# Optimization experiments

Hardware: AMD Instinct MI355X
Metric: run time of the kernel (lower is better)

The kernel has to match this reference:

```python
import jax, jax.numpy as jnp
import numpy as np

VOCAB = 128000
D = 256
N_BUBBLES = 256
N_EQ_STEPS = 5
SEQ_LEN = 512
ETA = 0.1      # relaxation rate toward input
KAPPA = 0.05   # mean-field coupling between bubbles


def setup_inputs() -> dict:
    key = jax.random.key(0)
    k1, k2, k3 = jax.random.split(key, 3)
    embed = jax.random.normal(k1, (VOCAB, D), dtype=jnp.float32)
    bubbles = jax.random.normal(k2, (N_BUBBLES, D), dtype=jnp.float32)
    memory_decay_base = jnp.asarray(0.8, dtype=jnp.float32)
    novelty_sensitivity = jnp.asarray(1.0, dtype=jnp.float32)
    tokens = jax.random.randint(k3, (SEQ_LEN,), 0, VOCAB, dtype=jnp.int64)
    return {"embed": embed, "bubbles": bubbles,
            "memory_decay_base": memory_decay_base,
            "novelty_sensitivity": novelty_sensitivity,
            "tokens": tokens}


def _foam_forward(x, bubbles):
    """x: [d]. Equilibrate bubble states, build density matrix, eigen-spectrum."""
    s = bubbles  # [n_bubbles, d]
    for _ in range(N_EQ_STEPS):  # fixed small hyperparam loop
        s = s + ETA * (x[None, :] - s) + KAPPA * (s.mean(axis=0, keepdims=True) - s)
        s = s / (jnp.linalg.norm(s, axis=-1, keepdims=True) + 1e-10)
    rho = (s.T @ s) / s.shape[0]  # [d, d] PSD, trace ~ 1
    w = jnp.linalg.eigvalsh(rho)  # ascending eigenvalues [d]
    w = jnp.clip(w, 0.0)
    output_dist = w / (w.sum() + 1e-10)
    return s, output_dist


def reference(embed, bubbles, memory_decay_base, novelty_sensitivity, tokens):
    sens = jnp.abs(novelty_sensitivity)

    def step(memory, tok):
        x = embed[tok]                      # [d]
        mem_mean = memory.mean(axis=0)      # [d]
        mem_norm = jnp.linalg.norm(mem_mean) + 1e-10
        x_norm = jnp.linalg.norm(x) + 1e-10
        novelty = jnp.where(mem_norm > 1e-8,
                            1.0 - jnp.dot(x, mem_mean) / (x_norm * mem_norm),
                            1.0)
        decay = jax.nn.sigmoid(memory_decay_base - sens * novelty)
        x_with_memory = x + decay * mem_mean
        eq, output_dist = _foam_forward(x_with_memory, bubbles)
        memory = decay * memory + (1.0 - decay) * eq
        return memory, output_dist

    memory0 = jnp.zeros_like(bubbles)  # [n_bubbles, d]
    _, dists = jax.lax.scan(step, memory0, tokens)
    return dists  # [seq_len, d] per-step eigenvalue distributions of rho
```

## Files before the change

### kernel.cpp

```cpp
#include <hip/hip_runtime.h>
#include <hip/hip_fp16.h>
#include <math.h>

#define SEQ 512
#define ETA 0.1f
#define KAPPA 0.05f
#define AA 0.85f

typedef _Float16 f16x8 __attribute__((ext_vector_type(8)));
typedef float f32x4 __attribute__((ext_vector_type(4)));

#define WS_G    ((size_t)0)
#define WS_GD   ((size_t)65536)
#define WS_M0   ((size_t)65792)
#define WS_BX   ((size_t)66048)
#define WS_X2   ((size_t)197120)
#define WS_ZS   ((size_t)197632)
#define WS_YS   ((size_t)328704)
#define WS_GS   ((size_t)459776)
#define WS_HS   ((size_t)984064)
#define WS_ALS  ((size_t)986112)
#define WS_BETS ((size_t)1117184)
#define WS_CT   ((size_t)1772544)

__device__ __forceinline__ float wred_sum(float v) {
#pragma unroll
  for (int m = 1; m < 64; m <<= 1) v += __shfl_xor(v, m, 64);
  return v;
}
__device__ __forceinline__ float wred_min(float v) {
#pragma unroll
  for (int m = 1; m < 64; m <<= 1) v = fminf(v, __shfl_xor(v, m, 64));
  return v;
}
__device__ __forceinline__ float wred_max(float v) {
#pragma unroll
  for (int m = 1; m < 64; m <<= 1) v = fmaxf(v, __shfl_xor(v, m, 64));
  return v;
}
__device__ __forceinline__ float rfl(float x) {
  return __builtin_bit_cast(float, __builtin_amdgcn_readfirstlane(__builtin_bit_cast(int, x)));
}

__global__ void k0_gram(const float* __restrict__ B, float* __restrict__ ws) {
  float* G = ws + WS_G;
  float* Gd = ws + WS_GD;
  __shared__ float bi[256];
  const int i = blockIdx.x, j = threadIdx.x;
  bi[j] = B[(size_t)i * 256 + j];
  __syncthreads();
  float a0 = 0.f, a1 = 0.f, a2 = 0.f, a3 = 0.f;
#pragma unroll
  for (int c = 0; c < 256; c += 4) {
    float4 b4 = *(const float4*)&B[(size_t)j * 256 + c];
    a0 = fmaf(bi[c + 0], b4.x, a0);
    a1 = fmaf(bi[c + 1], b4.y, a1);
    a2 = fmaf(bi[c + 2], b4.z, a2);
    a3 = fmaf(bi[c + 3], b4.w, a3);
  }
  float acc = (a0 + a1) + (a2 + a3);
  G[(size_t)i * 256 + j] = acc;
  if (i == j) Gd[i] = acc;
}

__global__ void k0_m0(const float* __restrict__ B, float* __restrict__ ws) {
  float* M0 = ws + WS_M0;
  const int d = threadIdx.x;
  float acc = 0.f;
  for (int i = 0; i < 256; ++i) acc += B[(size_t)i * 256 + d];
  M0[d] = acc * (1.0f / 256.0f);
}

__global__ void k0_bx(const float* __restrict__ B, const float* __restrict__ embed,
                      const int* __restrict__ toks, float* __restrict__ ws) {
  float* BX = ws + WS_BX;
  float* X2 = ws + WS_X2;
  __shared__ float xs[256];
  __shared__ float red[4];
  const int t = blockIdx.x, i = threadIdx.x;
  const int lane = i & 63, wid = i >> 6;
  const int tok = toks[t];
  float xv = embed[(size_t)tok * 256 + i];
  xs[i] = xv;
  float p = wred_sum(xv * xv);
  if (lane == 0) red[wid] = p;
  __syncthreads();
  if (i == 0) X2[t] = red[0] + red[1] + red[2] + red[3];
  float a0 = 0.f, a1 = 0.f, a2 = 0.f, a3 = 0.f;
#pragma unroll
  for (int c = 0; c < 256; c += 4) {
    float4 b4 = *(const float4*)&B[(size_t)i * 256 + c];
    a0 = fmaf(xs[c + 0], b4.x, a0);
    a1 = fmaf(xs[c + 1], b4.y, a1);
    a2 = fmaf(xs[c + 2], b4.z, a2);
    a3 = fmaf(xs[c + 3], b4.w, a3);
  }
  BX[(size_t)t * 256 + i] = (a0 + a1) + (a2 + a3);
}

__global__ __launch_bounds__(1024, 1) void k1_seq(
    const float* __restrict__ embed, const int* __restrict__ toks,
    const float* __restrict__ mdbp, const float* __restrict__ sensp,
    float* __restrict__ ws) {
  const int tid = threadIdx.x;
  const int lane = tid & 63;
  const int i = tid >> 2, h = tid & 3;
  const float* G = ws + WS_G;
  const float* Gd = ws + WS_GD;
  const float* BX = ws + WS_BX;
  const float* X2 = ws + WS_X2;
  float* ZS = ws + WS_ZS;
  float* YS = ws + WS_YS;
  float* GS = ws + WS_GS;
  float* HS = ws + WS_HS;
  float* ALS = ws + WS_ALS;
  float* BETS = ws + WS_BETS;

  __shared__ __align__(16) float gcur[4 * 68];
  __shared__ float dresb[2][8];
  __shared__ float bbarb[2][8];

  float4 Gq[16];
  {
    const float4* gp = (const float4*)(G + (size_t)i * 256 + (size_t)h * 64);
#pragma unroll
    for (int j = 0; j < 16; ++j) Gq[j] = gp[j];
  }
  const float Gdi = Gd[i];
  const float mdb = rfl(mdbp[0]);
  const float sens = fabsf(rfl(sensp[0]));

  float q0i;
  {
    float s = 0.f;
#pragma unroll
    for (int j = 0; j < 16; ++j) s += (Gq[j].x + Gq[j].y) + (Gq[j].z + Gq[j].w);
    s += __shfl_xor(s, 1, 64);
    s += __shfl_xor(s, 2, 64);
    q0i = s * (1.0f / 256.0f);
  }

  float x_c = embed[(size_t)toks[0] * 256 + i];
  float bx_c = BX[i];
  float x2_c = rfl(X2[0]);

  if (tid < 16) dresb[tid >> 3][tid & 7] = 0.f;
  else if (tid < 32) bbarb[(tid - 16) >> 3][tid & 7] = 0.f;
  __syncthreads();
  {
    float mv0 = 0.f;
    if (h == 0) mv0 = q0i * (1.0f / 256.0f);
    else if (h == 1) mv0 = bx_c * (1.0f / 256.0f);
#pragma unroll
    for (int m = 4; m <= 32; m <<= 1) mv0 += __shfl_xor(mv0, m, 64);
    if (lane < 2) atomicAdd(&dresb[0][lane], mv0);
  }
  __syncthreads();
  const float c00 = rfl(dresb[0][0]);
  float mbx = rfl(dresb[0][1]);

  float Zi = 0.f, yi = 0.f, wi = 0.f;
  float mm2 = 0.f, mw = 0.f, dotxm = 0.f;

  float dec = 1.0f / (1.0f + expf(-(mdb - sens)));
  float od = 1.0f - dec;
  float ri = bx_c;
  float XM2 = x2_c;
  float mean_r = mbx;
  if (h == 0) ZS[i] = 0.f;
  else if (h == 1) YS[i] = x_c;

  float gh[6], Ggh[6], hhv[6], bmat[5], xmm[5], alpha;
  gh[0] = 1.0f / 256.0f; Ggh[0] = q0i; hhv[0] = 0.f;
  {
    const float xmm0 = mean_r;
    const float tki = ETA * ri + KAPPA * q0i;
    const float CC00 = (ETA * ETA) * XM2 + 2.f * (ETA * KAPPA) * xmm0 +
                       (KAPPA * KAPPA) * c00;
    const float n2 = fmaxf(AA * AA * Gdi + 2.f * AA * tki + CC00, 0.f);
    const float inv = 1.0f / (sqrtf(n2) + 1e-10f);
    bmat[0] = inv; alpha = AA * inv; xmm[0] = xmm0;
  }
  if (h == 0) gcur[(i >> 6) * 68 + (i & 63)] = alpha;
  {
    float bv0 = (h == 0) ? bmat[0] : 0.f;
#pragma unroll
    for (int m = 4; m <= 32; m <<= 1) bv0 += __shfl_xor(bv0, m, 64);
    if (lane == 0) atomicAdd(&bbarb[1][0], bv0);
  }
  __syncthreads();
  int pq = 1;

#pragma unroll 1
  for (int t = 0; t < SEQ; ++t) {
    const int tn = (t + 1 < SEQ) ? (t + 1) : t;
    const int tokn = toks[tn];
    const float x_n = embed[(size_t)tokn * 256 + i];
    const float bx_n = BX[(size_t)tn * 256 + i];
    const float x2_n = rfl(X2[tn]);
    float q5sav = 0.f;

#pragma unroll
    for (int k = 1; k <= 5; ++k) {
      if (tid < 8) dresb[1 - pq][tid] = 0.f;
      else if (tid < 16) bbarb[1 - pq][tid - 8] = 0.f;
      float4 av = {0.f, 0.f, 0.f, 0.f};
      const float4* gc4 = (const float4*)&gcur[h * 68];
#pragma unroll
      for (int j = 0; j < 16; ++j) {
        const float4 g4 = gc4[j];
        av.x = fmaf(Gq[j].x, g4.x, av.x);
        av.y = fmaf(Gq[j].y, g4.y, av.y);
        av.z = fmaf(Gq[j].z, g4.z, av.z);
        av.w = fmaf(Gq[j].w, g4.w, av.w);
      }
      float M = (av.x + av.y) + (av.z + av.w);
      M += __shfl_xor(M, 1, 64);
      M += __shfl_xor(M, 2, 64);
      float hk = 0.f, gk = alpha * (1.0f / 256.0f), Ggk = M * (1.0f / 256.0f);
#pragma unroll
      for (int l = 0; l < 5; ++l)
        if (l < k) {
          const float bb = rfl(bbarb[pq][l]) * (1.0f / 256.0f);
          hk += bb * (ETA + KAPPA * hhv[l]);
          gk = fmaf(KAPPA * bb, gh[l], gk);
          Ggk = fmaf(KAPPA * bb, Ggh[l], Ggk);
        }
      const float qk = Ggk + hk * ri;
      gh[k] = gk; Ggh[k] = Ggk; hhv[k] = hk;
      if (k <= 4) {
        if (h == 2) GS[(size_t)(k - 1) * (SEQ * 256) + (size_t)t * 256 + i] = gk;
        if (tid == 0) HS[(size_t)(k - 1) * SEQ + t] = hk;
      }
      float vv[8];
      if (k < 5) {
#pragma unroll
        for (int l = 0; l < 8; ++l) {
          if (l <= k) vv[l] = gk * (Ggh[l] + hhv[l] * ri);
          else if (l == k + 1) vv[l] = ri * gk;
          else vv[l] = 0.f;
        }
      } else {
        q5sav = qk;
        vv[0] = gk * qk;
        vv[1] = ri * gk;
        vv[2] = wi * gk;
        vv[3] = qk * (1.0f / 256.0f);
        vv[4] = bx_n * Zi + x_n * yi;
        vv[5] = bx_n * gk;
        vv[6] = x_n * x_c;
        vv[7] = bx_n * (1.0f / 256.0f);
      }
      float mv0 = (h == 0) ? vv[0] : (h == 1) ? vv[1] : (h == 2) ? vv[2] : vv[3];
      float mv1 = (h == 0) ? vv[4] : (h == 1) ? vv[5] : (h == 2) ? vv[6] : vv[7];
#pragma unroll
      for (int m = 4; m <= 32; m <<= 1) {
        mv0 += __shfl_xor(mv0, m, 64);
        mv1 += __shfl_xor(mv1, m, 64);
      }
      const int nv = (k < 5) ? (k + 2) : 8;
      if (lane < 8 && lane < nv) atomicAdd(&dresb[pq][lane], lane < 4 ? mv0 : mv1);
      __syncthreads();

      if (k < 5) {
        float dres[7];
#pragma unroll
        for (int l = 0; l < 7; ++l)
          if (l <= k + 1) dres[l] = rfl(dresb[pq][l]);
        const float xmmk = dres[k + 1] + hk * XM2;
        const float tki = ETA * ri + KAPPA * qk;
        float sc = alpha * tki;
#pragma unroll
        for (int jj = 0; jj < 4; ++jj)
          if (jj < k) {
            const float MMjk = dres[jj] + hk * xmm[jj];
            const float CCjk = (ETA * ETA) * XM2 + (ETA * KAPPA) * (xmm[jj] + xmmk) +
                               (KAPPA * KAPPA) * MMjk;
            sc = fmaf(bmat[jj], CCjk, sc);
          }
        const float MMkk = dres[k] + hk * xmmk;
        const float CCkk = (ETA * ETA) * XM2 + 2.f * (ETA * KAPPA) * xmmk +
                           (KAPPA * KAPPA) * MMkk;
        const float n2 = fmaxf(AA * AA + 2.f * AA * sc + CCkk, 0.f);
        const float inv = 1.0f / (sqrtf(n2) + 1e-10f);
#pragma unroll
        for (int jj = 0; jj < 4; ++jj)
          if (jj < k) bmat[jj] *= AA * inv;
        bmat[k] = inv;
        alpha *= AA * inv;
        xmm[k] = xmmk;
        if (k == 4) {
          if (h == 3) ALS[(size_t)t * 256 + i] = alpha;
          if (h == 0) {
            BETS[(size_t)0 * (SEQ * 256) + (size_t)t * 256 + i] = bmat[0];
            BETS[(size_t)4 * (SEQ * 256) + (size_t)t * 256 + i] = bmat[4];
          } else if (h == 1) {
            BETS[(size_t)1 * (SEQ * 256) + (size_t)t * 256 + i] = bmat[1];
          } else if (h == 2) {
            BETS[(size_t)2 * (SEQ * 256) + (size_t)t * 256 + i] = bmat[2];
          } else {
            BETS[(size_t)3 * (SEQ * 256) + (size_t)t * 256 + i] = bmat[3];
          }
        }
        if (h == 0) gcur[(i >> 6) * 68 + (i & 63)] = alpha;
        float bv0 = (h == 0) ? bmat[0]
                  : (h == 1) ? ((k >= 1) ? bmat[1] : 0.f)
                  : (h == 2) ? ((k >= 2) ? bmat[2] : 0.f)
                             : ((k >= 3) ? bmat[3] : 0.f);
        float bv1 = (h == 0 && k >= 4) ? bmat[4] : 0.f;
#pragma unroll
        for (int m = 4; m <= 32; m <<= 1) {
          bv0 += __shfl_xor(bv0, m, 64);
          bv1 += __shfl_xor(bv1, m, 64);
        }
        if (lane < 8 && lane <= k)
          atomicAdd(&bbarb[1 - pq][lane], lane < 4 ? bv0 : bv1);
        __syncthreads();
        pq ^= 1;
      } else {
        float dr[8];
#pragma unroll
        for (int l = 0; l < 8; ++l) dr[l] = rfl(dresb[pq][l]);
        const float h5 = hhv[5];
        const float g5 = gh[5];
        const float q5 = q5sav;
        const float xmm5 = dr[1] + h5 * XM2;
        const float m52 = dr[0] + h5 * xmm5;
        const float cmm5 = dr[2] + h5 * (dotxm + dec * mm2);
        const float lamc = dec * (1.0f + od * h5);
        Zi = lamc * Zi + od * g5;
        yi = lamc * yi + od * h5 * x_c;
        wi = dec * wi + od * q5;
        mm2 = fmaxf(dec * dec * mm2 + 2.f * dec * od * cmm5 + od * od * m52, 0.f);
        mw = dec * mw + od * dr[3];
        dotxm = lamc * dr[4] + od * (dr[5] + h5 * dr[6]);
        mbx = dr[7];
        x_c = x_n; bx_c = bx_n; x2_c = x2_n;
        const float memnorm = sqrtf(mm2) + 1e-10f;
        const float xnorm = sqrtf(x2_c) + 1e-10f;
        const float nov = (memnorm > 1e-8f) ? (1.0f - dotxm / (xnorm * memnorm)) : 1.0f;
        dec = 1.0f / (1.0f + expf(-(mdb - sens * nov)));
        od = 1.0f - dec;
        ri = bx_c + dec * wi;
        XM2 = x2_c + 2.f * dec * dotxm + dec * dec * mm2;
        mean_r = mbx + dec * mw;
        if (t + 1 < SEQ) {
          if (h == 0) ZS[(size_t)(t + 1) * 256 + i] = dec * Zi;
          else if (h == 1) YS[(size_t)(t + 1) * 256 + i] = x_c + dec * yi;
        }
        const float xmm0 = mean_r;
        const float tki = ETA * ri + KAPPA * q0i;
        const float CC00 = (ETA * ETA) * XM2 + 2.f * (ETA * KAPPA) * xmm0 +
                           (KAPPA * KAPPA) * c00;
        const float n2 = fmaxf(AA * AA * Gdi + 2.f * AA * tki + CC00, 0.f);
        const float inv = 1.0f / (sqrtf(n2) + 1e-10f);
        bmat[0] = inv; alpha = AA * inv; xmm[0] = xmm0;
        if (h == 0) gcur[(i >> 6) * 68 + (i & 63)] = alpha;
        float bv0 = (h == 0) ? bmat[0] : 0.f;
#pragma unroll
        for (int m = 4; m <= 32; m <<= 1) bv0 += __shfl_xor(bv0, m, 64);
        if (lane == 0) atomicAdd(&bbarb[1 - pq][0], bv0);
        __syncthreads();
        pq ^= 1;
      }
    }
  }
}

__global__ void k15_cvec(const float* __restrict__ B, float* __restrict__ ws) {
  const float* ZS = ws + WS_ZS;
  const float* YS = ws + WS_YS;
  const float* GS = ws + WS_GS;
  const float* HS = ws + WS_HS;
  const float* M0 = ws + WS_M0;
  float* CT = ws + WS_CT;
  const int t = blockIdx.x, d = threadIdx.x;
  __shared__ float zs[256], g1[256], g2[256], g3[256], g4[256];
  zs[d] = ZS[(size_t)t * 256 + d];
  g1[d] = GS[0 * (SEQ * 256) + (size_t)t * 256 + d];
  g2[d] = GS[1 * (SEQ * 256) + (size_t)t * 256 + d];
  g3[d] = GS[2 * (SEQ * 256) + (size_t)t * 256 + d];
  g4[d] = GS[3 * (SEQ * 256) + (size_t)t * 256 + d];
  __syncthreads();
  float xa = 0.f, b1 = 0.f, b2 = 0.f, b3 = 0.f, b4 = 0.f;
  for (int ii = 0; ii < 256; ++ii) {
    const float Bv = B[(size_t)ii * 256 + d];
    xa = fmaf(zs[ii], Bv, xa);
    b1 = fmaf(g1[ii], Bv, b1);
    b2 = fmaf(g2[ii], Bv, b2);
    b3 = fmaf(g3[ii], Bv, b3);
    b4 = fmaf(g4[ii], Bv, b4);
  }
  const float xm = YS[(size_t)t * 256 + d] + xa;
  float* ctt = CT + (size_t)t * 1280;
  ctt[0 * 256 + d] = ETA * xm + KAPPA * M0[d];
  const float h1 = HS[0 * SEQ + t], h2 = HS[1 * SEQ + t];
  const float h3 = HS[2 * SEQ + t], h4 = HS[3 * SEQ + t];
  ctt[1 * 256 + d] = (ETA + KAPPA * h1) * xm + KAPPA * b1;
  ctt[2 * 256 + d] = (ETA + KAPPA * h2) * xm + KAPPA * b2;
  ctt[3 * 256 + d] = (ETA + KAPPA * h3) * xm + KAPPA * b3;
  ctt[4 * 256 + d] = (ETA + KAPPA * h4) * xm + KAPPA * b4;
}

__global__ __launch_bounds__(1024, 4) void k2_eig(
    const float* __restrict__ B, const float* __restrict__ ws,
    float* __restrict__ out) {
  const int t = blockIdx.x;
  const int tid = threadIdx.x;
  const int lane = tid & 63, wid = tid >> 6;
  const float* CT = ws + WS_CT + (size_t)t * 1280;
  const float* ALS = ws + WS_ALS + (size_t)t * 256;
  const float* BETS = ws + WS_BETS;

  __shared__ __align__(16) unsigned char bigbuf[135168];
  _Float16* sT = (_Float16*)bigbuf;
  float* pk = (float*)bigbuf;
  __shared__ __align__(16) float ct[1280];
  __shared__ float vx[256], pv[256], qv[256];
  __shared__ float dd[256], ee[256], e2[256], lamv[256];
  __shared__ float red[16];

  for (int idx = tid; idx < 1280; idx += 1024) ct[idx] = CT[idx];
  __syncthreads();

  {
    const int r = tid >> 2, q = tid & 3;
    const float al = ALS[r];
    const float be0 = BETS[(size_t)0 * (SEQ * 256) + (size_t)t * 256 + r];
    const float be1 = BETS[(size_t)1 * (SEQ * 256) + (size_t)t * 256 + r];
    const float be2 = BETS[(size_t)2 * (SEQ * 256) + (size_t)t * 256 + r];
    const float be3 = BETS[(size_t)3 * (SEQ * 256) + (size_t)t * 256 + r];
    const float be4 = BETS[(size_t)4 * (SEQ * 256) + (size_t)t * 256 + r];
#pragma unroll
    for (int j4 = 0; j4 < 16; ++j4) {
      const int d0 = q * 64 + j4 * 4;
      const float4 Bv = *(const float4*)&B[(size_t)r * 256 + d0];
      const float4 c0 = *(const float4*)&ct[0 * 256 + d0];
      const float4 c1 = *(const float4*)&ct[1 * 256 + d0];
      const float4 c2 = *(const float4*)&ct[2 * 256 + d0];
      const float4 c3 = *(const float4*)&ct[3 * 256 + d0];
      const float4 c4 = *(const float4*)&ct[4 * 256 + d0];
      const float s0 = al * Bv.x + be0 * c0.x + be1 * c1.x + be2 * c2.x + be3 * c3.x + be4 * c4.x;
      const float s1 = al * Bv.y + be0 * c0.y + be1 * c1.y + be2 * c2.y + be3 * c3.y + be4 * c4.y;
      const float s2 = al * Bv.z + be0 * c0.z + be1 * c1.z + be2 * c2.z + be3 * c3.z + be4 * c4.z;
      const float s3 = al * Bv.w + be0 * c0.w + be1 * c1.w + be2 * c2.w + be3 * c3.w + be4 * c4.w;
      sT[(size_t)(d0 + 0) * 264 + r] = (_Float16)s0;
      sT[(size_t)(d0 + 1) * 264 + r] = (_Float16)s1;
      sT[(size_t)(d0 + 2) * 264 + r] = (_Float16)s2;
      sT[(size_t)(d0 + 3) * 264 + r] = (_Float16)s3;
    }
  }
  __syncthreads();

  f32x4 acc[4][4];
#pragma unroll
  for (int ti = 0; ti < 4; ++ti)
#pragma unroll
    for (int tj = 0; tj < 4; ++tj) {
      f32x4 z = {0.f, 0.f, 0.f, 0.f};
      acc[ti][tj] = z;
    }
  {
    const int Ib = (wid >> 2) * 4, Jb = (wid & 3) * 4;
    const int mr = lane & 15, kg = lane >> 4;
#pragma unroll 1
    for (int kb = 0; kb < 8; ++kb) {
      const int ko = kb * 32 + kg * 8;
      f16x8 aF[4], bF[4];
#pragma unroll
      for (int ti = 0; ti < 4; ++ti)
        aF[ti] = *(const f16x8*)&sT[(size_t)((Ib + ti) * 16 + mr) * 264 + ko];
#pragma unroll
      for (int tj = 0; tj < 4; ++tj)
        bF[tj] = *(const f16x8*)&sT[(size_t)((Jb + tj) * 16 + mr) * 264 + ko];
#pragma unroll
      for (int ti = 0; ti < 4; ++ti)
#pragma unroll
        for (int tj = 0; tj < 4; ++tj)
          acc[ti][tj] = __builtin_amdgcn_mfma_f32_16x16x32_f16(aF[ti], bF[tj], acc[ti][tj], 0, 0, 0);
    }
  }
  __syncthreads();
  {
    const int Ib = (wid >> 2) * 4, Jb = (wid & 3) * 4;
    const int cn = lane & 15, rg = lane >> 4;
#pragma unroll
    for (int ti = 0; ti < 4; ++ti)
#pragma unroll
      for (int tj = 0; tj < 4; ++tj) {
        const int C = (Jb + tj) * 16 + cn;
        const int Rb = (Ib + ti) * 16 + rg * 4;
#pragma unroll
        for (int rr = 0; rr < 4; ++rr) {
          const int R = Rb + rr;
          if (R >= C) pk[R * (R + 1) / 2 + C] = acc[ti][tj][rr] * (1.0f / 256.0f);
        }
      }
  }
  __syncthreads();

#pragma unroll 1
  for (int j = 0; j < 254; ++j) {
    const int m = 255 - j;
    const float x0 = pk[(j + 1) * (j + 2) / 2 + j];
    float ps = 0.f;
    if (tid < m) {
      const int gr = j + 1 + tid;
      const float xv_ = pk[gr * (gr + 1) / 2 + j];
      vx[tid] = xv_;
      ps = xv_ * xv_;
    }
    ps = wred_sum(ps);
    if (lane == 0) red[wid] = ps;
    __syncthreads();
    float sig2 = 0.f;
#pragma unroll
    for (int w = 0; w < 16; ++w) sig2 += red[w];
    const float sig = sqrtf(sig2);
    const float sg = (x0 >= 0.f) ? 1.f : -1.f;
    const bool live = (sig2 > 1e-26f);
    const float beta = live ? (1.0f / (sig * (sig + fabsf(x0)))) : 0.f;
    const float v0 = live ? (x0 + sg * sig) : 0.f;
    if (tid == 0) {
      dd[j] = pk[j * (j + 1) / 2 + j];
      ee[j] = live ? (-sg * sig) : x0;
      vx[0] = v0;
    }
    __syncthreads();
    {
      const int ri_ = tid >> 2, qd = tid & 3;
      float acc2 = 0.f;
      if (ri_ < m) {
        const int gr = j + 1 + ri_;
        const int c0 = (m * qd) >> 2, c1 = (m * (qd + 1)) >> 2;
        const int rowbase = gr * (gr + 1) / 2 + (j + 1);
        const int clend = min(c1, ri_ + 1);
        for (int c = c0; c < clend; ++c) acc2 = fmaf(pk[rowbase + c], vx[c], acc2);
        const int cu = max(c0, ri_ + 1);
        if (cu < c1) {
          int gc = j + 1 + cu;
          int ub = gc * (gc + 1) / 2 + gr;
          int stp = gc + 1;
          for (int c = cu; c < c1; ++c) { acc2 = fmaf(pk[ub], vx[c], acc2); ub += stp; ++stp; }
        }
      }
      acc2 += __shfl_xor(acc2, 1, 64);
      acc2 += __shfl_xor(acc2, 2, 64);
      float vpp = 0.f;
      if ((tid & 3) == 0 && (tid >> 2) < m) { pv[tid >> 2] = acc2; vpp = acc2 * vx[tid >> 2]; }
      vpp = wred_sum(vpp);
      if (lane == 0) red[wid] = vpp;
    }
    __syncthreads();
    float vtp = 0.f;
#pragma unroll
    for (int w = 0; w < 16; ++w) vtp += red[w];
    const float gamma = 0.5f * beta * beta * vtp;
    if (tid < m) qv[tid] = beta * pv[tid] - gamma * vx[tid];
    __syncthreads();
    {
      const int Q = tid >> 2, qd = tid & 3;
      const int i2 = m - 1 - Q;
      if (Q <= i2 && Q < m) {
        {
          const int gr = j + 1 + Q;
          const int rb = gr * (gr + 1) / 2 + (j + 1);
          const float vi = vx[Q], qi = qv[Q];
          const int cs = (qd * (Q + 1)) >> 2, ce = ((qd + 1) * (Q + 1)) >> 2;
          for (int c = cs; c < ce; ++c) pk[rb + c] -= vi * qv[c] + qi * vx[c];
        }
        if (i2 > Q) {
          const int gr = j + 1 + i2;
          const int rb = gr * (gr + 1) / 2 + (j + 1);
          const float vi = vx[i2], qi = qv[i2];
          const int cs = (qd * (i2 + 1)) >> 2, ce = ((qd + 1) * (i2 + 1)) >> 2;
          for (int c = cs; c < ce; ++c) pk[rb + c] -= vi * qv[c] + qi * vx[c];
        }
      }
    }
    __syncthreads();
  }
  if (tid == 0) {
    dd[254] = pk[254 * 255 / 2 + 254];
    dd[255] = pk[255 * 256 / 2 + 255];
    ee[254] = pk[255 * 256 / 2 + 254];
    ee[255] = 0.f;
  }
  __syncthreads();
  if (tid < 256) e2[tid] = ee[tid] * ee[tid];
  __syncthreads();
  float glo = 1e30f, ghi = -1e30f;
  if (tid < 256) {
    const float rad = fabsf(ee[tid]) + ((tid > 0) ? fabsf(ee[tid - 1]) : 0.f);
    glo = dd[tid] - rad;
    ghi = dd[tid] + rad;
  }
  {
    float v = wred_min(glo);
    if (lane == 0) red[wid] = v;
    __syncthreads();
    float lo0 = 1e30f;
#pragma unroll
    for (int w = 0; w < 16; ++w) lo0 = fminf(lo0, red[w]);
    __syncthreads();
    v = wred_max(ghi);
    if (lane == 0) red[wid] = v;
    __syncthreads();
    float hi0 = -1e30f;
#pragma unroll
    for (int w = 0; w < 16; ++w) hi0 = fmaxf(hi0, red[w]);
    lo0 -= 1e-3f + 1e-3f * fabsf(lo0);
    hi0 += 1e-3f + 1e-3f * fabsf(hi0);
    if (tid < 256) {
      float lo = lo0, hi = hi0;
      for (int it = 0; it < 21; ++it) {
        const float x = 0.5f * (lo + hi);
        int cnt = 0;
        float qq = dd[0] - x;
        cnt += (qq < 0.f);
        for (int ii = 1; ii < 256; ++ii) {
          float dn = qq;
          if (fabsf(dn) < 1e-25f) dn = (dn < 0.f) ? -1e-25f : 1e-25f;
          qq = (dd[ii] - x) - e2[ii - 1] * __builtin_amdgcn_rcpf(dn);
          cnt += (qq < 0.f);
        }
        if (cnt >= tid + 1) hi = x; else lo = x;
      }
      lamv[tid] = fmaxf(0.5f * (lo + hi), 0.f);
    }
  }
  __syncthreads();
  float sv = (tid < 256) ? lamv[tid] : 0.f;
  sv = wred_sum(sv);
  if (lane == 0) red[wid] = sv;
  __syncthreads();
  float S = 0.f;
#pragma unroll
  for (int w = 0; w < 16; ++w) S += red[w];
  if (tid < 256) out[(size_t)t * 256 + tid] = lamv[tid] / (S + 1e-10f);
}

extern "C" void kernel_launch(void* const* d_in, const int* in_sizes, int n_in,
                              void* d_out, int out_size, void* d_ws, size_t ws_size,
                              hipStream_t stream) {
  const float* embed = (const float*)d_in[0];
  const float* B = (const float*)d_in[1];
  const float* mdb = (const float*)d_in[2];
  const float* sens = (const float*)d_in[3];
  const int* toks = (const int*)d_in[4];
  float* out = (float*)d_out;
  float* ws = (float*)d_ws;

  k0_gram<<<dim3(256), dim3(256), 0, stream>>>(B, ws);
  k0_m0<<<dim3(1), dim3(256), 0, stream>>>(B, ws);
  k0_bx<<<dim3(SEQ), dim3(256), 0, stream>>>(B, embed, toks, ws);
  k1_seq<<<dim3(1), dim3(1024), 0, stream>>>(embed, toks, mdb, sens, ws);
  k15_cvec<<<dim3(SEQ), dim3(256), 0, stream>>>(B, ws);
  k2_eig<<<dim3(SEQ), dim3(1024), 0, stream>>>(B, ws, out);
}
```

Before: 12.01 ms.

## Halve sequential kernel block to 512 threads with two lanes per row

The single-block sequential recurrence kernel now runs 512 threads, with each row of the Gram matrix split across 2 threads instead of 4. Each thread holds 32 float4 registers of G, named through a macro so they stay in registers. This removes one shuffle level and cuts the number of waves taking part in each barrier. Reductions are rewritten as 32-lane partial sums whose results are combined with atomics. The cost is higher register pressure and more serial FMA work per thread in the matrix-vector product.

```diff
diff --git a/kernel.cpp b/kernel.cpp
--- a/kernel.cpp
+++ b/kernel.cpp
@@ -38,9 +38,22 @@
   for (int m = 1; m < 64; m <<= 1) v = fmaxf(v, __shfl_xor(v, m, 64));
   return v;
 }
+__device__ __forceinline__ float psum32(float v) {
+  v += __shfl_xor(v, 2, 64);
+  v += __shfl_xor(v, 4, 64);
+  v += __shfl_xor(v, 8, 64);
+  v += __shfl_xor(v, 16, 64);
+  v += __shfl_xor(v, 32, 64);
+  return v;
+}
 __device__ __forceinline__ float rfl(float x) {
   return __builtin_bit_cast(float, __builtin_amdgcn_readfirstlane(__builtin_bit_cast(int, x)));
 }
+
+#define G_LIST(X) X(0) X(1) X(2) X(3) X(4) X(5) X(6) X(7) \
+                  X(8) X(9) X(10) X(11) X(12) X(13) X(14) X(15) \
+                  X(16) X(17) X(18) X(19) X(20) X(21) X(22) X(23) \
+                  X(24) X(25) X(26) X(27) X(28) X(29) X(30) X(31)
 
 __global__ void k0_gram(const float* __restrict__ B, float* __restrict__ ws) {
   float* G = ws + WS_G;
@@ -98,13 +111,15 @@
   BX[(size_t)t * 256 + i] = (a0 + a1) + (a2 + a3);
 }
 
-__global__ __launch_bounds__(1024, 1) void k1_seq(
+__global__ __launch_bounds__(512)
+__attribute__((amdgpu_waves_per_eu(2, 2)))
+void k1_seq(
     const float* __restrict__ embed, const int* __restrict__ toks,
     const float* __restrict__ mdbp, const float* __restrict__ sensp,
     float* __restrict__ ws) {
   const int tid = threadIdx.x;
   const int lane = tid & 63;
-  const int i = tid >> 2, h = tid & 3;
+  const int i = tid >> 1, h = tid & 1;
   const float* G = ws + WS_G;
   const float* Gd = ws + WS_GD;
   const float* BX = ws + WS_BX;
@@ -116,16 +131,14 @@
   float* ALS = ws + WS_ALS;
   float* BETS = ws + WS_BETS;
 
-  __shared__ __align__(16) float gcur[4 * 68];
+  __shared__ __align__(16) float gcur[256];
   __shared__ float dresb[2][8];
   __shared__ float bbarb[2][8];
 
-  float4 Gq[16];
-  {
-    const float4* gp = (const float4*)(G + (size_t)i * 256 + (size_t)h * 64);
-#pragma unroll
-    for (int j = 0; j < 16; ++j) Gq[j] = gp[j];
-  }
+  const float4* gp = (const float4*)(G + (size_t)i * 256 + (size_t)h * 128);
+#define DECLG(J) float4 Gr##J = gp[J];
+  G_LIST(DECLG)
+#undef DECLG
   const float Gdi = Gd[i];
   const float mdb = rfl(mdbp[0]);
   const float sens = fabsf(rfl(sensp[0]));
@@ -133,10 +146,10 @@
   float q0i;
   {
     float s = 0.f;
-#pragma unroll
-    for (int j = 0; j < 16; ++j) s += (Gq[j].x + Gq[j].y) + (Gq[j].z + Gq[j].w);
+#define SUMG(J) s += (Gr##J.x + Gr##J.y) + (Gr##J.z + Gr##J.w);
+    G_LIST(SUMG)
+#undef SUMG
     s += __shfl_xor(s, 1, 64);
-    s += __shfl_xor(s, 2, 64);
     q0i = s * (1.0f / 256.0f);
   }
 
@@ -148,12 +161,9 @@
   else if (tid < 32) bbarb[(tid - 16) >> 3][tid & 7] = 0.f;
   __syncthreads();
   {
-    float mv0 = 0.f;
-    if (h == 0) mv0 = q0i * (1.0f / 256.0f);
-    else if (h == 1) mv0 = bx_c * (1.0f / 256.0f);
-#pragma unroll
-    for (int m = 4; m <= 32; m <<= 1) mv0 += __shfl_xor(mv0, m, 64);
-    if (lane < 2) atomicAdd(&dresb[0][lane], mv0);
+    float v = h ? (bx_c * (1.0f / 256.0f)) : (q0i * (1.0f / 256.0f));
+    v = psum32(v);
+    if (lane == h) atomicAdd(&dresb[0][h], v);
   }
   __syncthreads();
   const float c00 = rfl(dresb[0][0]);
@@ -168,7 +178,7 @@
   float XM2 = x2_c;
   float mean_r = mbx;
   if (h == 0) ZS[i] = 0.f;
-  else if (h == 1) YS[i] = x_c;
+  else YS[i] = x_c;
 
   float gh[6], Ggh[6], hhv[6], bmat[5], xmm[5], alpha;
   gh[0] = 1.0f / 256.0f; Ggh[0] = q0i; hhv[0] = 0.f;
@@ -181,12 +191,11 @@
     const float inv = 1.0f / (sqrtf(n2) + 1e-10f);
     bmat[0] = inv; alpha = AA * inv; xmm[0] = xmm0;
   }
-  if (h == 0) gcur[(i >> 6) * 68 + (i & 63)] = alpha;
-  {
-    float bv0 = (h == 0) ? bmat[0] : 0.f;
-#pragma unroll
-    for (int m = 4; m <= 32; m <<= 1) bv0 += __shfl_xor(bv0, m, 64);
-    if (lane == 0) atomicAdd(&bbarb[1][0], bv0);
+  if (h == 0) gcur[i] = alpha;
+  {
+    float bv = h ? 0.f : bmat[0];
+    bv = psum32(bv);
+    if (lane == 0) atomicAdd(&bbarb[1][0], bv);
   }
   __syncthreads();
   int pq = 1;
@@ -205,18 +214,14 @@
       if (tid < 8) dresb[1 - pq][tid] = 0.f;
       else if (tid < 16) bbarb[1 - pq][tid - 8] = 0.f;
       float4 av = {0.f, 0.f, 0.f, 0.f};
-      const float4* gc4 = (const float4*)&gcur[h * 68];
-#pragma unroll
-      for (int j = 0; j < 16; ++j) {
-        const float4 g4 = gc4[j];
-        av.x = fmaf(Gq[j].x, g4.x, av.x);
-        av.y = fmaf(Gq[j].y, g4.y, av.y);
-        av.z = fmaf(Gq[j].z, g4.z, av.z);
-        av.w = fmaf(Gq[j].w, g4.w, av.w);
-      }
+      const float4* gc4 = (const float4*)&gcur[h * 128];
+#define MVG(J) { const float4 g4 = gc4[J]; \
+      av.x = fmaf(Gr##J.x, g4.x, av.x); av.y = fmaf(Gr##J.y, g4.y, av.y); \
+      av.z = fmaf(Gr##J.z, g4.z, av.z); av.w = fmaf(Gr##J.w, g4.w, av.w); }
+      G_LIST(MVG)
+#undef MVG
       float M = (av.x + av.y) + (av.z + av.w);
       M += __shfl_xor(M, 1, 64);
-      M += __shfl_xor(M, 2, 64);
       float hk = 0.f, gk = alpha * (1.0f / 256.0f), Ggk = M * (1.0f / 256.0f);
 #pragma unroll
       for (int l = 0; l < 5; ++l)
@@ -229,7 +234,7 @@
       const float qk = Ggk + hk * ri;
       gh[k] = gk; Ggh[k] = Ggk; hhv[k] = hk;
       if (k <= 4) {
-        if (h == 2) GS[(size_t)(k - 1) * (SEQ * 256) + (size_t)t * 256 + i] = gk;
+        if (h == 1) GS[(size_t)(k - 1) * (SEQ * 256) + (size_t)t * 256 + i] = gk;
         if (tid == 0) HS[(size_t)(k - 1) * SEQ + t] = hk;
       }
       float vv[8];
@@ -251,15 +256,19 @@
         vv[6] = x_n * x_c;
         vv[7] = bx_n * (1.0f / 256.0f);
       }
-      float mv0 = (h == 0) ? vv[0] : (h == 1) ? vv[1] : (h == 2) ? vv[2] : vv[3];
-      float mv1 = (h == 0) ? vv[4] : (h == 1) ? vv[5] : (h == 2) ? vv[6] : vv[7];
-#pragma unroll
-      for (int m = 4; m <= 32; m <<= 1) {
-        mv0 += __shfl_xor(mv0, m, 64);
-        mv1 += __shfl_xor(mv1, m, 64);
-      }
       const int nv = (k < 5) ? (k + 2) : 8;
-      if (lane < 8 && lane < nv) atomicAdd(&dresb[pq][lane], lane < 4 ? mv0 : mv1);
+      const int ulim = (k < 5) ? (k + 2) : 4;
+      float red4[4] = {0.f, 0.f, 0.f, 0.f};
+#pragma unroll
+      for (int u = 0; u < 4; ++u)
+        if (u < ulim) red4[u] = psum32(h ? vv[4 + u] : vv[u]);
+      if (lane == h) {
+#pragma unroll
+        for (int u = 0; u < 4; ++u) {
+          const int sl = h * 4 + u;
+          if (sl < nv) atomicAdd(&dresb[pq][sl], red4[u]);
+        }
+      }
       __syncthreads();
 
       if (k < 5) {
@@ -290,31 +299,28 @@
         alpha *= AA * inv;
         xmm[k] = xmmk;
         if (k == 4) {
-          if (h == 3) ALS[(size_t)t * 256 + i] = alpha;
-          if (h == 0) {
+          if (h == 1) {
+            ALS[(size_t)t * 256 + i] = alpha;
+            BETS[(size_t)1 * (SEQ * 256) + (size_t)t * 256 + i] = bmat[1];
+            BETS[(size_t)3 * (SEQ * 256) + (size_t)t * 256 + i] = bmat[3];
+          } else {
             BETS[(size_t)0 * (SEQ * 256) + (size_t)t * 256 + i] = bmat[0];
+            BETS[(size_t)2 * (SEQ * 256) + (size_t)t * 256 + i] = bmat[2];
             BETS[(size_t)4 * (SEQ * 256) + (size_t)t * 256 + i] = bmat[4];
-          } else if (h == 1) {
-            BETS[(size_t)1 * (SEQ * 256) + (size_t)t * 256 + i] = bmat[1];
-          } else if (h == 2) {
-            BETS[(size_t)2 * (SEQ * 256) + (size_t)t * 256 + i] = bmat[2];
-          } else {
-            BETS[(size_t)3 * (SEQ * 256) + (size_t)t * 256 + i] = bmat[3];
           }
         }
-        if (h == 0) gcur[(i >> 6) * 68 + (i & 63)] = alpha;
-        float bv0 = (h == 0) ? bmat[0]
-                  : (h == 1) ? ((k >= 1) ? bmat[1] : 0.f)
-                  : (h == 2) ? ((k >= 2) ? bmat[2] : 0.f)
-                             : ((k >= 3) ? bmat[3] : 0.f);
-        float bv1 = (h == 0 && k >= 4) ? bmat[4] : 0.f;
-#pragma unroll
-        for (int m = 4; m <= 32; m <<= 1) {
-          bv0 += __shfl_xor(bv0, m, 64);
-          bv1 += __shfl_xor(bv1, m, 64);
-        }
-        if (lane < 8 && lane <= k)
-          atomicAdd(&bbarb[1 - pq][lane], lane < 4 ? bv0 : bv1);
+        if (h == 0) gcur[i] = alpha;
+        float rb0 = h ? bmat[1] : bmat[0];
+        float rb1 = h ? ((k >= 3) ? bmat[3] : 0.f) : ((k >= 2) ? bmat[2] : 0.f);
+        float rb2 = h ? 0.f : ((k >= 4) ? bmat[4] : 0.f);
+        rb0 = psum32(rb0);
+        if (k >= 2) rb1 = psum32(rb1);
+        if (k >= 4) rb2 = psum32(rb2);
+        if (lane == h) {
+          atomicAdd(&bbarb[1 - pq][h], rb0);
+          if (2 + h <= k) atomicAdd(&bbarb[1 - pq][2 + h], rb1);
+          if (4 + h <= k) atomicAdd(&bbarb[1 - pq][4 + h], rb2);
+        }
         __syncthreads();
         pq ^= 1;
       } else {
@@ -346,7 +352,7 @@
         mean_r = mbx + dec * mw;
         if (t + 1 < SEQ) {
           if (h == 0) ZS[(size_t)(t + 1) * 256 + i] = dec * Zi;
-          else if (h == 1) YS[(size_t)(t + 1) * 256 + i] = x_c + dec * yi;
+          else YS[(size_t)(t + 1) * 256 + i] = x_c + dec * yi;
         }
         const float xmm0 = mean_r;
         const float tki = ETA * ri + KAPPA * q0i;
@@ -355,11 +361,10 @@
         const float n2 = fmaxf(AA * AA * Gdi + 2.f * AA * tki + CC00, 0.f);
         const float inv = 1.0f / (sqrtf(n2) + 1e-10f);
         bmat[0] = inv; alpha = AA * inv; xmm[0] = xmm0;
-        if (h == 0) gcur[(i >> 6) * 68 + (i & 63)] = alpha;
-        float bv0 = (h == 0) ? bmat[0] : 0.f;
-#pragma unroll
-        for (int m = 4; m <= 32; m <<= 1) bv0 += __shfl_xor(bv0, m, 64);
-        if (lane == 0) atomicAdd(&bbarb[1 - pq][0], bv0);
+        if (h == 0) gcur[i] = alpha;
+        float bv = h ? 0.f : bmat[0];
+        bv = psum32(bv);
+        if (lane == 0) atomicAdd(&bbarb[1 - pq][0], bv);
         __syncthreads();
         pq ^= 1;
       }
@@ -654,7 +659,7 @@
   k0_gram<<<dim3(256), dim3(256), 0, stream>>>(B, ws);
   k0_m0<<<dim3(1), dim3(256), 0, stream>>>(B, ws);
   k0_bx<<<dim3(SEQ), dim3(256), 0, stream>>>(B, embed, toks, ws);
-  k1_seq<<<dim3(1), dim3(1024), 0, stream>>>(embed, toks, mdb, sens, ws);
+  k1_seq<<<dim3(1), dim3(512), 0, stream>>>(embed, toks, mdb, sens, ws);
   k15_cvec<<<dim3(SEQ), dim3(256), 0, stream>>>(B, ws);
   k2_eig<<<dim3(SEQ), dim3(1024), 0, stream>>>(B, ws, out);
 }
```

Result: faster. 10.63 ms (-11.5%).
